# Optimization experiments

Hardware: AMD Instinct MI355X
Metric: run time of the kernel (lower is better)

## Reference

```python
import jax, jax.numpy as jnp
import numpy as np

RADIX = 16
INPUT_SIZE = 4096  # 16**3 -> 3 recursion levels
# residual flags per level, replicating the source quirk:
# level0: residual=True -> bool(True)=True, passes int(True)-1 = 0
# level1: residual=0    -> bool(0)=False,   passes int(0)-1   = -1
# level2: residual=-1   -> bool(-1)=True (negative ints are truthy)
RES_FLAGS = (True, False, True)


def _butterfly(x, weights, lins, res_flags):
    """Faithful vectorized translation of OptimisedRNNFFT.forward.

    x: (..., N); weights: list of per-level vectors (N, N/r, ...);
    lins: list of (radix, radix) matrices; res_flags: per-level residual bools.
    """
    n = x.shape[-1]
    chunk = n // RADIX
    if n > RADIX:
        # recurse on radix-sized chunks of the last dim
        xr = x.reshape(*x.shape[:-1], RADIX, chunk)
        y = _butterfly(xr, weights[1:], lins[1:], res_flags[1:])
        y = y.reshape(*x.shape[:-1], n)
    else:
        y = x  # Identity at the base level
    y = weights[0] * y                                   # elementwise weighting
    yb = y.reshape(*y.shape[:-1], RADIX, chunk)          # (..., radix, chunk)
    r = jnp.einsum('ij,...jc->...ic', lins[0], yb)       # radix x radix mix
    r = r.reshape(*y.shape[:-1], n)
    if res_flags[0]:
        r = r + x
    return r


def setup_inputs() -> dict:
    key = jax.random.key(0)
    k = jax.random.split(key, 8)
    x = jax.random.normal(k[0], (8192, INPUT_SIZE), dtype=jnp.float32)
    # per-level elementwise weights (torch init: ones/sqrt(N); randomized here)
    w0 = jax.random.normal(k[1], (4096,), dtype=jnp.float32) / np.sqrt(4096.0)
    w1 = jax.random.normal(k[2], (256,), dtype=jnp.float32) / np.sqrt(256.0)
    w2 = jax.random.normal(k[3], (16,), dtype=jnp.float32) / np.sqrt(16.0)
    # per-level radix x radix butterfly matrices (xavier-normal-ish)
    xav = np.sqrt(2.0 / (RADIX + RADIX))
    l0 = jax.random.normal(k[4], (RADIX, RADIX), dtype=jnp.float32) * xav
    l1 = jax.random.normal(k[5], (RADIX, RADIX), dtype=jnp.float32) * xav
    l2 = jax.random.normal(k[6], (RADIX, RADIX), dtype=jnp.float32) * xav
    return {"x": x, "w0": w0, "w1": w1, "w2": w2, "l0": l0, "l1": l1, "l2": l2}


def reference(x, w0, w1, w2, l0, l1, l2):
    return _butterfly(x, [w0, w1, w2], [l0, l1, l2], RES_FLAGS)
```

## Files before the change

kernel.cpp:

```cpp
#include <hip/hip_runtime.h>

#define N 4096

__global__ __launch_bounds__(256, 4) void butterfly3_kernel(
    const float* __restrict__ x,
    const float* __restrict__ w0, const float* __restrict__ w1, const float* __restrict__ w2,
    const float* __restrict__ l0, const float* __restrict__ l1, const float* __restrict__ l2,
    float* __restrict__ out)
{
    __shared__ float2 lds[N + (N >> 4)];
    const int t = threadIdx.x;
    const int b1 = t >> 4, c1 = t & 15;
    const size_t row0 = (size_t)blockIdx.x * 2;
    const float* __restrict__ xA = x + row0 * N;
    const float* __restrict__ xB = xA + N;
    float* __restrict__ oA = out + row0 * N;
    float* __restrict__ oB = oA + N;

    float vA[16], vB[16];
    {
        const float4* qA = (const float4*)(xA + t * 16);
        const float4* qB = (const float4*)(xB + t * 16);
        float4 fa0 = qA[0], fa1 = qA[1], fa2 = qA[2], fa3 = qA[3];
        float4 fb0 = qB[0], fb1 = qB[1], fb2 = qB[2], fb3 = qB[3];
        vA[0]=fa0.x; vA[1]=fa0.y; vA[2]=fa0.z; vA[3]=fa0.w;
        vA[4]=fa1.x; vA[5]=fa1.y; vA[6]=fa1.z; vA[7]=fa1.w;
        vA[8]=fa2.x; vA[9]=fa2.y; vA[10]=fa2.z; vA[11]=fa2.w;
        vA[12]=fa3.x; vA[13]=fa3.y; vA[14]=fa3.z; vA[15]=fa3.w;
        vB[0]=fb0.x; vB[1]=fb0.y; vB[2]=fb0.z; vB[3]=fb0.w;
        vB[4]=fb1.x; vB[5]=fb1.y; vB[6]=fb1.z; vB[7]=fb1.w;
        vB[8]=fb2.x; vB[9]=fb2.y; vB[10]=fb2.z; vB[11]=fb2.w;
        vB[12]=fb3.x; vB[13]=fb3.y; vB[14]=fb3.z; vB[15]=fb3.w;
    }

    float xwA[16], xwB[16];
    #pragma unroll
    for (int j = 0; j < 16; ++j) {
        float s = w2[j];
        xwA[j] = s * vA[j];
        xwB[j] = s * vB[j];
    }
    #pragma unroll
    for (int i = 0; i < 16; ++i) {
        float a = vA[i], b = vB[i];
        #pragma unroll
        for (int j = 0; j < 16; ++j) {
            float s = l2[i*16 + j];
            a = fmaf(s, xwA[j], a);
            b = fmaf(s, xwB[j], b);
        }
        lds[t*17 + i] = make_float2(a, b);
    }

    float w1c[16];
    #pragma unroll
    for (int j = 0; j < 16; ++j) w1c[j] = w1[j*16 + c1];

    float2 y1[16];
    #pragma unroll
    for (int j = 0; j < 16; ++j) {
        float2 p = lds[b1*272 + j*17 + c1];
        y1[j].x = w1c[j] * p.x;
        y1[j].y = w1c[j] * p.y;
    }
    #pragma unroll
    for (int i = 0; i < 16; ++i) {
        float a = 0.f, b = 0.f;
        #pragma unroll
        for (int j = 0; j < 16; ++j) {
            float s = l1[i*16 + j];
            a = fmaf(s, y1[j].x, a);
            b = fmaf(s, y1[j].y, b);
        }
        lds[b1*272 + i*17 + c1] = make_float2(a, b);
    }

    __syncthreads();

    float w0c[16], xrA[16], xrB[16];
    #pragma unroll
    for (int j = 0; j < 16; ++j) w0c[j] = w0[j*256 + t];
    #pragma unroll
    for (int i = 0; i < 16; ++i) { xrA[i] = xA[i*256 + t]; xrB[i] = xB[i*256 + t]; }

    const int tb = t + (t >> 4);
    float2 y0[16];
    #pragma unroll
    for (int j = 0; j < 16; ++j) {
        float2 p = lds[j*272 + tb];
        y0[j].x = w0c[j] * p.x;
        y0[j].y = w0c[j] * p.y;
    }
    #pragma unroll
    for (int i = 0; i < 16; ++i) {
        float a = xrA[i], b = xrB[i];
        #pragma unroll
        for (int j = 0; j < 16; ++j) {
            float s = l0[i*16 + j];
            a = fmaf(s, y0[j].x, a);
            b = fmaf(s, y0[j].y, b);
        }
        oA[i*256 + t] = a;
        oB[i*256 + t] = b;
    }
}

extern "C" void kernel_launch(void* const* d_in, const int* in_sizes, int n_in,
                              void* d_out, int out_size, void* d_ws, size_t ws_size,
                              hipStream_t stream) {
    const float* x  = (const float*)d_in[0];
    const float* w0 = (const float*)d_in[1];
    const float* w1 = (const float*)d_in[2];
    const float* w2 = (const float*)d_in[3];
    const float* l0 = (const float*)d_in[4];
    const float* l1 = (const float*)d_in[5];
    const float* l2 = (const float*)d_in[6];
    float* out = (float*)d_out;
    const int rows = in_sizes[0] / N;
    butterfly3_kernel<<<rows / 2, 256, 0, stream>>>(x, w0, w1, w2, l0, l1, l2, out);
}
```

Baseline: 69.22 us.

## Make butterfly kernel persistent with next-pair prefetch and XOR-swizzled LDS

```diff
diff --git a/kernel.cpp b/kernel.cpp
--- a/kernel.cpp
+++ b/kernel.cpp
@@ -1,107 +1,127 @@
 #include <hip/hip_runtime.h>
 
 #define N 4096
+#define GRID 1024
 
-__global__ __launch_bounds__(256, 4) void butterfly3_kernel(
+__device__ __forceinline__ int swz(int e) { return e ^ ((e >> 4) & 15); }
+
+__global__ __launch_bounds__(256, 4) void butterfly4_kernel(
     const float* __restrict__ x,
     const float* __restrict__ w0, const float* __restrict__ w1, const float* __restrict__ w2,
     const float* __restrict__ l0, const float* __restrict__ l1, const float* __restrict__ l2,
-    float* __restrict__ out)
+    float* __restrict__ out, int pairs)
 {
-    __shared__ float2 lds[N + (N >> 4)];
+    __shared__ float2 lds[N];
     const int t = threadIdx.x;
     const int b1 = t >> 4, c1 = t & 15;
-    const size_t row0 = (size_t)blockIdx.x * 2;
-    const float* __restrict__ xA = x + row0 * N;
-    const float* __restrict__ xB = xA + N;
-    float* __restrict__ oA = out + row0 * N;
-    float* __restrict__ oB = oA + N;
+
+    float w1c[16], w0c[16];
+    #pragma unroll
+    for (int j = 0; j < 16; ++j) w1c[j] = w1[j*16 + c1];
+    #pragma unroll
+    for (int j = 0; j < 16; ++j) w0c[j] = w0[j*256 + t];
 
     float vA[16], vB[16];
     {
-        const float4* qA = (const float4*)(xA + t * 16);
-        const float4* qB = (const float4*)(xB + t * 16);
-        float4 fa0 = qA[0], fa1 = qA[1], fa2 = qA[2], fa3 = qA[3];
-        float4 fb0 = qB[0], fb1 = qB[1], fb2 = qB[2], fb3 = qB[3];
-        vA[0]=fa0.x; vA[1]=fa0.y; vA[2]=fa0.z; vA[3]=fa0.w;
-        vA[4]=fa1.x; vA[5]=fa1.y; vA[6]=fa1.z; vA[7]=fa1.w;
-        vA[8]=fa2.x; vA[9]=fa2.y; vA[10]=fa2.z; vA[11]=fa2.w;
-        vA[12]=fa3.x; vA[13]=fa3.y; vA[14]=fa3.z; vA[15]=fa3.w;
-        vB[0]=fb0.x; vB[1]=fb0.y; vB[2]=fb0.z; vB[3]=fb0.w;
-        vB[4]=fb1.x; vB[5]=fb1.y; vB[6]=fb1.z; vB[7]=fb1.w;
-        vB[8]=fb2.x; vB[9]=fb2.y; vB[10]=fb2.z; vB[11]=fb2.w;
-        vB[12]=fb3.x; vB[13]=fb3.y; vB[14]=fb3.z; vB[15]=fb3.w;
+        const float4* qA = (const float4*)(x + (size_t)blockIdx.x*2*N + t*16);
+        const float4* qB = (const float4*)(x + ((size_t)blockIdx.x*2+1)*N + t*16);
+        #pragma unroll
+        for (int q = 0; q < 4; ++q) {
+            float4 f = qA[q];
+            vA[q*4+0]=f.x; vA[q*4+1]=f.y; vA[q*4+2]=f.z; vA[q*4+3]=f.w;
+        }
+        #pragma unroll
+        for (int q = 0; q < 4; ++q) {
+            float4 f = qB[q];
+            vB[q*4+0]=f.x; vB[q*4+1]=f.y; vB[q*4+2]=f.z; vB[q*4+3]=f.w;
+        }
     }
 
-    float xwA[16], xwB[16];
-    #pragma unroll
-    for (int j = 0; j < 16; ++j) {
-        float s = w2[j];
-        xwA[j] = s * vA[j];
-        xwB[j] = s * vB[j];
-    }
-    #pragma unroll
-    for (int i = 0; i < 16; ++i) {
-        float a = vA[i], b = vB[i];
+    for (int p = blockIdx.x; p < pairs; p += GRID) {
+        const float* __restrict__ xA = x + (size_t)p*2*N;
+        const float* __restrict__ xB = xA + N;
+        float* __restrict__ oA = out + (size_t)p*2*N;
+        float* __restrict__ oB = oA + N;
+
+        float xwA[16], xwB[16];
+        #pragma unroll
+        for (int j = 0; j < 16; ++j) { float s = w2[j]; xwA[j]=s*vA[j]; xwB[j]=s*vB[j]; }
+        #pragma unroll
+        for (int i = 0; i < 16; ++i) {
+            float a = vA[i], b = vB[i];
+            #pragma unroll
+            for (int j = 0; j < 16; ++j) {
+                float s = l2[i*16+j];
+                a = fmaf(s, xwA[j], a);
+                b = fmaf(s, xwB[j], b);
+            }
+            lds[swz(t*16 + i)] = make_float2(a, b);
+        }
+
+        float2 y1[16];
         #pragma unroll
         for (int j = 0; j < 16; ++j) {
-            float s = l2[i*16 + j];
-            a = fmaf(s, xwA[j], a);
-            b = fmaf(s, xwB[j], b);
+            float2 q = lds[swz(b1*256 + j*16 + c1)];
+            y1[j].x = w1c[j]*q.x; y1[j].y = w1c[j]*q.y;
         }
-        lds[t*17 + i] = make_float2(a, b);
-    }
+        #pragma unroll
+        for (int i = 0; i < 16; ++i) {
+            float a = 0.f, b = 0.f;
+            #pragma unroll
+            for (int j = 0; j < 16; ++j) {
+                float s = l1[i*16+j];
+                a = fmaf(s, y1[j].x, a);
+                b = fmaf(s, y1[j].y, b);
+            }
+            lds[swz(b1*256 + i*16 + c1)] = make_float2(a, b);
+        }
 
-    float w1c[16];
-    #pragma unroll
-    for (int j = 0; j < 16; ++j) w1c[j] = w1[j*16 + c1];
+        __syncthreads();
 
-    float2 y1[16];
-    #pragma unroll
-    for (int j = 0; j < 16; ++j) {
-        float2 p = lds[b1*272 + j*17 + c1];
-        y1[j].x = w1c[j] * p.x;
-        y1[j].y = w1c[j] * p.y;
-    }
-    #pragma unroll
-    for (int i = 0; i < 16; ++i) {
-        float a = 0.f, b = 0.f;
+        float2 y0[16];
         #pragma unroll
         for (int j = 0; j < 16; ++j) {
-            float s = l1[i*16 + j];
-            a = fmaf(s, y1[j].x, a);
-            b = fmaf(s, y1[j].y, b);
+            float2 q = lds[swz(j*256 + t)];
+            y0[j].x = w0c[j]*q.x; y0[j].y = w0c[j]*q.y;
         }
-        lds[b1*272 + i*17 + c1] = make_float2(a, b);
-    }
 
-    __syncthreads();
+        __syncthreads();
 
-    float w0c[16], xrA[16], xrB[16];
-    #pragma unroll
-    for (int j = 0; j < 16; ++j) w0c[j] = w0[j*256 + t];
-    #pragma unroll
-    for (int i = 0; i < 16; ++i) { xrA[i] = xA[i*256 + t]; xrB[i] = xB[i*256 + t]; }
+        const bool more = (p + GRID) < pairs;
+        float pA[16], pB[16];
+        if (more) {
+            const float4* nA = (const float4*)(xA + (size_t)GRID*2*N + t*16);
+            const float4* nB = (const float4*)(xB + (size_t)GRID*2*N + t*16);
+            #pragma unroll
+            for (int q = 0; q < 4; ++q) {
+                float4 f = nA[q];
+                pA[q*4+0]=f.x; pA[q*4+1]=f.y; pA[q*4+2]=f.z; pA[q*4+3]=f.w;
+            }
+            #pragma unroll
+            for (int q = 0; q < 4; ++q) {
+                float4 f = nB[q];
+                pB[q*4+0]=f.x; pB[q*4+1]=f.y; pB[q*4+2]=f.z; pB[q*4+3]=f.w;
+            }
+        }
 
-    const int tb = t + (t >> 4);
-    float2 y0[16];
-    #pragma unroll
-    for (int j = 0; j < 16; ++j) {
-        float2 p = lds[j*272 + tb];
-        y0[j].x = w0c[j] * p.x;
-        y0[j].y = w0c[j] * p.y;
-    }
-    #pragma unroll
-    for (int i = 0; i < 16; ++i) {
-        float a = xrA[i], b = xrB[i];
         #pragma unroll
-        for (int j = 0; j < 16; ++j) {
-            float s = l0[i*16 + j];
-            a = fmaf(s, y0[j].x, a);
-            b = fmaf(s, y0[j].y, b);
+        for (int i = 0; i < 16; ++i) {
+            float a = xA[i*256 + t];
+            float b = xB[i*256 + t];
+            #pragma unroll
+            for (int j = 0; j < 16; ++j) {
+                float s = l0[i*16+j];
+                a = fmaf(s, y0[j].x, a);
+                b = fmaf(s, y0[j].y, b);
+            }
+            oA[i*256 + t] = a;
+            oB[i*256 + t] = b;
         }
-        oA[i*256 + t] = a;
-        oB[i*256 + t] = b;
+
+        if (more) {
+            #pragma unroll
+            for (int k = 0; k < 16; ++k) { vA[k] = pA[k]; vB[k] = pB[k]; }
+        }
     }
 }
 
@@ -116,6 +136,6 @@
     const float* l1 = (const float*)d_in[5];
     const float* l2 = (const float*)d_in[6];
     float* out = (float*)d_out;
-    const int rows = in_sizes[0] / N;
-    butterfly3_kernel<<<rows / 2, 256, 0, stream>>>(x, w0, w1, w2, l0, l1, l2, out);
+    const int pairs = (in_sizes[0] / N) / 2;
+    butterfly4_kernel<<<GRID, 256, 0, stream>>>(x, w0, w1, w2, l0, l1, l2, out, pairs);
 }
```

Measured after the change: 200.0 us. 189% more time.

## Swizzle LDS layout, raise occupancy bound, and use nontemporal output stores

Applied to the files above, without the earlier changes.

```diff
diff --git a/kernel.cpp b/kernel.cpp
--- a/kernel.cpp
+++ b/kernel.cpp
@@ -2,13 +2,15 @@
 
 #define N 4096
 
-__global__ __launch_bounds__(256, 4) void butterfly3_kernel(
+__device__ __forceinline__ int swz(int e) { return e ^ ((e >> 4) & 15); }
+
+__global__ __launch_bounds__(256, 6) void butterfly5_kernel(
     const float* __restrict__ x,
     const float* __restrict__ w0, const float* __restrict__ w1, const float* __restrict__ w2,
     const float* __restrict__ l0, const float* __restrict__ l1, const float* __restrict__ l2,
     float* __restrict__ out)
 {
-    __shared__ float2 lds[N + (N >> 4)];
+    __shared__ float2 lds[N];
     const int t = threadIdx.x;
     const int b1 = t >> 4, c1 = t & 15;
     const size_t row0 = (size_t)blockIdx.x * 2;
@@ -21,16 +23,16 @@
     {
         const float4* qA = (const float4*)(xA + t * 16);
         const float4* qB = (const float4*)(xB + t * 16);
-        float4 fa0 = qA[0], fa1 = qA[1], fa2 = qA[2], fa3 = qA[3];
-        float4 fb0 = qB[0], fb1 = qB[1], fb2 = qB[2], fb3 = qB[3];
-        vA[0]=fa0.x; vA[1]=fa0.y; vA[2]=fa0.z; vA[3]=fa0.w;
-        vA[4]=fa1.x; vA[5]=fa1.y; vA[6]=fa1.z; vA[7]=fa1.w;
-        vA[8]=fa2.x; vA[9]=fa2.y; vA[10]=fa2.z; vA[11]=fa2.w;
-        vA[12]=fa3.x; vA[13]=fa3.y; vA[14]=fa3.z; vA[15]=fa3.w;
-        vB[0]=fb0.x; vB[1]=fb0.y; vB[2]=fb0.z; vB[3]=fb0.w;
-        vB[4]=fb1.x; vB[5]=fb1.y; vB[6]=fb1.z; vB[7]=fb1.w;
-        vB[8]=fb2.x; vB[9]=fb2.y; vB[10]=fb2.z; vB[11]=fb2.w;
-        vB[12]=fb3.x; vB[13]=fb3.y; vB[14]=fb3.z; vB[15]=fb3.w;
+        #pragma unroll
+        for (int q = 0; q < 4; ++q) {
+            float4 f = qA[q];
+            vA[q*4+0]=f.x; vA[q*4+1]=f.y; vA[q*4+2]=f.z; vA[q*4+3]=f.w;
+        }
+        #pragma unroll
+        for (int q = 0; q < 4; ++q) {
+            float4 f = qB[q];
+            vB[q*4+0]=f.x; vB[q*4+1]=f.y; vB[q*4+2]=f.z; vB[q*4+3]=f.w;
+        }
     }
 
     float xwA[16], xwB[16];
@@ -49,7 +51,7 @@
             a = fmaf(s, xwA[j], a);
             b = fmaf(s, xwB[j], b);
         }
-        lds[t*17 + i] = make_float2(a, b);
+        lds[swz(t*16 + i)] = make_float2(a, b);
     }
 
     float w1c[16];
@@ -59,10 +61,11 @@
     float2 y1[16];
     #pragma unroll
     for (int j = 0; j < 16; ++j) {
-        float2 p = lds[b1*272 + j*17 + c1];
+        float2 p = lds[swz(b1*256 + j*16 + c1)];
         y1[j].x = w1c[j] * p.x;
         y1[j].y = w1c[j] * p.y;
     }
+    float2 r1[16];
     #pragma unroll
     for (int i = 0; i < 16; ++i) {
         float a = 0.f, b = 0.f;
@@ -72,10 +75,11 @@
             a = fmaf(s, y1[j].x, a);
             b = fmaf(s, y1[j].y, b);
         }
-        lds[b1*272 + i*17 + c1] = make_float2(a, b);
+        r1[i] = make_float2(a, b);
     }
-
-    __syncthreads();
+    #pragma unroll
+    for (int i = 0; i < 16; ++i)
+        lds[swz(b1*256 + i*16 + c1)] = r1[i];
 
     float w0c[16], xrA[16], xrB[16];
     #pragma unroll
@@ -83,11 +87,12 @@
     #pragma unroll
     for (int i = 0; i < 16; ++i) { xrA[i] = xA[i*256 + t]; xrB[i] = xB[i*256 + t]; }
 
-    const int tb = t + (t >> 4);
+    __syncthreads();
+
     float2 y0[16];
     #pragma unroll
     for (int j = 0; j < 16; ++j) {
-        float2 p = lds[j*272 + tb];
+        float2 p = lds[swz(j*256 + t)];
         y0[j].x = w0c[j] * p.x;
         y0[j].y = w0c[j] * p.y;
     }
@@ -100,8 +105,8 @@
             a = fmaf(s, y0[j].x, a);
             b = fmaf(s, y0[j].y, b);
         }
-        oA[i*256 + t] = a;
-        oB[i*256 + t] = b;
+        __builtin_nontemporal_store(a, &oA[i*256 + t]);
+        __builtin_nontemporal_store(b, &oB[i*256 + t]);
     }
 }
 
@@ -117,5 +122,5 @@
     const float* l2 = (const float*)d_in[6];
     float* out = (float*)d_out;
     const int rows = in_sizes[0] / N;
-    butterfly3_kernel<<<rows / 2, 256, 0, stream>>>(x, w0, w1, w2, l0, l1, l2, out);
+    butterfly5_kernel<<<rows / 2, 256, 0, stream>>>(x, w0, w1, w2, l0, l1, l2, out);
 }
```

After: 68.93 us. About the same (-0.4%).
